# Performance work log

Hardware: AMD Instinct MI355X
Metric: run time of the kernel (lower is better)

Reference implementation:

```python
import jax, jax.numpy as jnp
import numpy as np

DIM_INPUT = 100000
DIM_LATENT = 128
NNZ = 819200
BATCH = 16384


def setup_inputs() -> dict:
    key = jax.random.key(0)
    k1, k2, k3, k4, k5 = jax.random.split(key, 5)
    vals = jax.random.uniform(k1, (NNZ,), dtype=jnp.float32)
    row_idx = jnp.sort(jax.random.randint(k2, (NNZ,), 0, BATCH, dtype=jnp.int32))
    col_idx = jax.random.randint(k3, (NNZ,), 0, DIM_INPUT, dtype=jnp.int32)
    # learned parameters (match torch init: w0 zeros, w/v randn)
    w0 = jnp.zeros((1,), dtype=jnp.float32)
    w = jax.random.normal(k4, (DIM_INPUT,), dtype=jnp.float32)
    v = jax.random.normal(k5, (DIM_INPUT, DIM_LATENT), dtype=jnp.float32)
    return {"vals": vals, "row_idx": row_idx, "col_idx": col_idx,
            "batch": BATCH, "w0": w0, "w": w, "v": v}


def reference(vals, row_idx, col_idx, batch, w0, w, v):
    # x is a sparse [batch, dim_input] matrix in COO form (row_idx, col_idx, vals).
    # linear term: w0 + x @ w
    linear = w0[0] + jax.ops.segment_sum(vals * w[col_idx], row_idx,
                                         num_segments=batch)
    # gather latent rows once: [nnz, K]
    v_rows = v[col_idx]
    weighted = vals[:, None] * v_rows                      # [nnz, K]
    xv = jax.ops.segment_sum(weighted, row_idx, num_segments=batch)       # [B, K]
    x_v_sq = jax.ops.segment_sum(weighted * v_rows, row_idx,
                                 num_segments=batch)       # x @ (v**2): [B, K]
    interaction = 0.5 * (jnp.sum(xv * xv, axis=1) - jnp.sum(x_v_sq, axis=1))
    return linear + interaction
```

## Files before the change

kernel.cpp:

```cpp
#include <hip/hip_runtime.h>

#define FM_NNZ   819200
#define FM_BATCH 16384
#define FM_DIM   100000
#define FM_K     128
#define WAVES    4
#define BATCH    16


static __device__ __forceinline__ uint32_t f2bf(float f) {
    uint32_t u = __float_as_uint(f);
    return (u + 0x7fffu + ((u >> 16) & 1u)) >> 16;
}

__global__ __launch_bounds__(256) void cvt_kernel(const float* __restrict__ v,
                                                  uint32_t* __restrict__ vb) {
    const float4* __restrict__ v4 = (const float4*)v;
    uint2* __restrict__ o = (uint2*)vb;
    const int n = (FM_DIM * FM_K) / 4;
    for (int i = blockIdx.x * blockDim.x + threadIdx.x; i < n;
         i += gridDim.x * blockDim.x) {
        const float4 x = v4[i];
        uint2 r;
        r.x = f2bf(x.x) | (f2bf(x.y) << 16);
        r.y = f2bf(x.z) | (f2bf(x.w) << 16);
        o[i] = r;
    }
}


__global__ __launch_bounds__(256) void fm_fwd_kernel(
    const float* __restrict__ vals,
    const int*   __restrict__ row_idx,
    const int*   __restrict__ col_idx,
    const float* __restrict__ w0,
    const float* __restrict__ w,
    const uint32_t* __restrict__ vb,
    float*       __restrict__ out)
{
    const int wave = threadIdx.x >> 6;
    const int lane = threadIdx.x & 63;
    const int row  = blockIdx.x * WAVES + wave;

    int lo = 0, hi = FM_NNZ;
    while (lo < hi) {
        int mid = (lo + hi) >> 1;
        if (row_idx[mid] < row) lo = mid + 1; else hi = mid;
    }
    const int start = lo;
    hi = FM_NNZ;
    while (lo < hi) {
        int mid = (lo + hi) >> 1;
        if (row_idx[mid] < row + 1) lo = mid + 1; else hi = mid;
    }
    const int end = lo;

    float xv_lo = 0.f, xv_hi = 0.f;
    float sq_lo = 0.f, sq_hi = 0.f;
    float lin = 0.f;

    for (int base = start; base < end; base += 64) {
        const int cnt = min(64, end - base);

        const int idxc = min(base + lane, FM_NNZ - 1);
        const int   c  = col_idx[idxc];
        const float a  = (lane < cnt) ? vals[idxc] : 0.f;

        lin = fmaf(a, w[c], lin);

        int j = 0;
        for (; j + BATCH <= cnt; j += BATCH) {
            uint32_t vv[BATCH];
            float    aa[BATCH];
            #pragma unroll
            for (int u = 0; u < BATCH; ++u) {
                const int cj = __shfl(c, j + u);
                aa[u] = __shfl(a, j + u);
                vv[u] = vb[(size_t)cj * 64 + lane];
            }
            #pragma unroll
            for (int u = 0; u < BATCH; ++u) {
                const float vlo = __uint_as_float(vv[u] << 16);
                const float vhi = __uint_as_float(vv[u] & 0xffff0000u);
                const float tl = aa[u] * vlo;
                const float th = aa[u] * vhi;
                xv_lo += tl;  xv_hi += th;
                sq_lo = fmaf(tl, vlo, sq_lo);
                sq_hi = fmaf(th, vhi, sq_hi);
            }
        }
        for (; j < cnt; ++j) {
            const int   cj = __shfl(c, j);
            const float aj = __shfl(a, j);
            const uint32_t u = vb[(size_t)cj * 64 + lane];
            const float vlo = __uint_as_float(u << 16);
            const float vhi = __uint_as_float(u & 0xffff0000u);
            const float tl = aj * vlo;
            const float th = aj * vhi;
            xv_lo += tl;  xv_hi += th;
            sq_lo = fmaf(tl, vlo, sq_lo);
            sq_hi = fmaf(th, vhi, sq_hi);
        }
    }

    float part = xv_lo * xv_lo + xv_hi * xv_hi - sq_lo - sq_hi;
    #pragma unroll
    for (int off = 32; off > 0; off >>= 1) {
        part += __shfl_down(part, off);
        lin  += __shfl_down(lin,  off);
    }
    if (lane == 0) {
        out[row] = w0[0] + lin + 0.5f * part;
    }
}

extern "C" void kernel_launch(void* const* d_in, const int* in_sizes, int n_in,
                              void* d_out, int out_size, void* d_ws, size_t ws_size,
                              hipStream_t stream) {
    const float* vals    = (const float*)d_in[0];
    const int*   row_idx = (const int*)  d_in[1];
    const int*   col_idx = (const int*)  d_in[2];
    const float* w0      = (const float*)d_in[4];
    const float* w       = (const float*)d_in[5];
    const float* v       = (const float*)d_in[6];
    float*       out     = (float*)d_out;
    uint32_t*    vb      = (uint32_t*)d_ws;

    cvt_kernel<<<1024, 256, 0, stream>>>(v, vb);
    fm_fwd_kernel<<<FM_BATCH / WAVES, 64 * WAVES, 0, stream>>>(
        vals, row_idx, col_idx, w0, w, vb, out);
}
```

Baseline: 165.4 us.

## Split wave into four 16-lane groups loading 16-byte bf16 rows per nonzero

```diff
diff --git a/kernel.cpp b/kernel.cpp
--- a/kernel.cpp
+++ b/kernel.cpp
@@ -5,7 +5,7 @@
 #define FM_DIM   100000
 #define FM_K     128
 #define WAVES    4
-#define BATCH    16
+#define UNR      8
 
 
 static __device__ __forceinline__ uint32_t f2bf(float f) {
@@ -40,6 +40,8 @@
 {
     const int wave = threadIdx.x >> 6;
     const int lane = threadIdx.x & 63;
+    const int grp  = lane >> 4;
+    const int ql   = lane & 15;
     const int row  = blockIdx.x * WAVES + wave;
 
     int lo = 0, hi = FM_NNZ;
@@ -55,8 +57,10 @@
     }
     const int end = lo;
 
-    float xv_lo = 0.f, xv_hi = 0.f;
-    float sq_lo = 0.f, sq_hi = 0.f;
+    const uint4* __restrict__ vb4 = (const uint4*)vb;
+
+    float xv[8] = {0.f,0.f,0.f,0.f,0.f,0.f,0.f,0.f};
+    float sq[8] = {0.f,0.f,0.f,0.f,0.f,0.f,0.f,0.f};
     float lin = 0.f;
 
     for (int base = start; base < end; base += 64) {
@@ -68,42 +72,51 @@
 
         lin = fmaf(a, w[c], lin);
 
-        int j = 0;
-        for (; j + BATCH <= cnt; j += BATCH) {
-            uint32_t vv[BATCH];
-            float    aa[BATCH];
+        for (int j = 0; j < cnt; j += 4 * UNR) {
+            uint4 vv[UNR];
+            float aa[UNR];
             #pragma unroll
-            for (int u = 0; u < BATCH; ++u) {
-                const int cj = __shfl(c, j + u);
-                aa[u] = __shfl(a, j + u);
-                vv[u] = vb[(size_t)cj * 64 + lane];
+            for (int u = 0; u < UNR; ++u) {
+                const int g  = j + 4 * u + grp;
+                const int gc = min(g, cnt - 1);
+                const float av = __shfl(a, gc);
+                const int   cj = __shfl(c, gc);
+                aa[u] = (g < cnt) ? av : 0.f;
+                vv[u] = vb4[(size_t)cj * 16 + ql];
             }
+            __builtin_amdgcn_sched_barrier(0);
             #pragma unroll
-            for (int u = 0; u < BATCH; ++u) {
-                const float vlo = __uint_as_float(vv[u] << 16);
-                const float vhi = __uint_as_float(vv[u] & 0xffff0000u);
-                const float tl = aa[u] * vlo;
-                const float th = aa[u] * vhi;
-                xv_lo += tl;  xv_hi += th;
-                sq_lo = fmaf(tl, vlo, sq_lo);
-                sq_hi = fmaf(th, vhi, sq_hi);
+            for (int u = 0; u < UNR; ++u) {
+                const float au = aa[u];
+                const uint32_t wds[4] = {vv[u].x, vv[u].y, vv[u].z, vv[u].w};
+                #pragma unroll
+                for (int q = 0; q < 4; ++q) {
+                    const float vlo = __uint_as_float(wds[q] << 16);
+                    const float vhi = __uint_as_float(wds[q] & 0xffff0000u);
+                    const float tl  = au * vlo;
+                    const float th  = au * vhi;
+                    xv[2*q]   += tl;
+                    xv[2*q+1] += th;
+                    sq[2*q]   = fmaf(tl, vlo, sq[2*q]);
+                    sq[2*q+1] = fmaf(th, vhi, sq[2*q+1]);
+                }
             }
-        }
-        for (; j < cnt; ++j) {
-            const int   cj = __shfl(c, j);
-            const float aj = __shfl(a, j);
-            const uint32_t u = vb[(size_t)cj * 64 + lane];
-            const float vlo = __uint_as_float(u << 16);
-            const float vhi = __uint_as_float(u & 0xffff0000u);
-            const float tl = aj * vlo;
-            const float th = aj * vhi;
-            xv_lo += tl;  xv_hi += th;
-            sq_lo = fmaf(tl, vlo, sq_lo);
-            sq_hi = fmaf(th, vhi, sq_hi);
         }
     }
 
-    float part = xv_lo * xv_lo + xv_hi * xv_hi - sq_lo - sq_hi;
+    float px = 0.f;
+    #pragma unroll
+    for (int d = 0; d < 8; ++d) {
+        float t = xv[d];
+        t += __shfl_xor(t, 16);
+        t += __shfl_xor(t, 32);
+        px = fmaf(t, t, px);
+    }
+    float sqs = 0.f;
+    #pragma unroll
+    for (int d = 0; d < 8; ++d) sqs += sq[d];
+
+    float part = ((lane < 16) ? px : 0.f) - sqs;
     #pragma unroll
     for (int off = 32; off > 0; off >>= 1) {
         part += __shfl_down(part, off);
```

Measured after the change: 174.9 us. +5.7%, slower.

## Walk column-bucketed nonzeros so concurrent waves share L2-resident latent rows

Applied to the files above, without the earlier changes.

```diff
diff --git a/kernel.cpp b/kernel.cpp
--- a/kernel.cpp
+++ b/kernel.cpp
@@ -4,8 +4,9 @@
 #define FM_BATCH 16384
 #define FM_DIM   100000
 #define FM_K     128
-#define WAVES    4
-#define BATCH    16
+#define NB_SHIFT 13
+#define NBUCK    13
+#define BAD_COL  (1 << 20)
 
 
 static __device__ __forceinline__ uint32_t f2bf(float f) {
@@ -29,88 +30,88 @@
 }
 
 
-__global__ __launch_bounds__(256) void fm_fwd_kernel(
+__global__ __launch_bounds__(256, 8) void fm_fwd_kernel(
     const float* __restrict__ vals,
     const int*   __restrict__ row_idx,
     const int*   __restrict__ col_idx,
     const float* __restrict__ w0,
-    const float* __restrict__ w,
+    const float* __restrict__ w_,
     const uint32_t* __restrict__ vb,
     float*       __restrict__ out)
 {
     const int wave = threadIdx.x >> 6;
     const int lane = threadIdx.x & 63;
-    const int row  = blockIdx.x * WAVES + wave;
+    const int wid  = blockIdx.x * 4 + wave;
+    const int row0 = 2 * wid;
+    const int row1 = row0 + 1;
 
-    int lo = 0, hi = FM_NNZ;
-    while (lo < hi) {
-        int mid = (lo + hi) >> 1;
-        if (row_idx[mid] < row) lo = mid + 1; else hi = mid;
+    int s[3];
+    #pragma unroll
+    for (int q = 0; q < 3; ++q) {
+        const int key = row0 + q;
+        int lo = 0, hi = FM_NNZ;
+        while (lo < hi) {
+            const int mid = (lo + hi) >> 1;
+            if (row_idx[mid] < key) lo = mid + 1; else hi = mid;
+        }
+        s[q] = lo;
     }
-    const int start = lo;
-    hi = FM_NNZ;
-    while (lo < hi) {
-        int mid = (lo + hi) >> 1;
-        if (row_idx[mid] < row + 1) lo = mid + 1; else hi = mid;
-    }
-    const int end = lo;
+    const int s0 = s[0], s1 = s[1], s2 = s[2];
 
-    float xv_lo = 0.f, xv_hi = 0.f;
-    float sq_lo = 0.f, sq_hi = 0.f;
-    float lin = 0.f;
-
-    for (int base = start; base < end; base += 64) {
-        const int cnt = min(64, end - base);
-
-        const int idxc = min(base + lane, FM_NNZ - 1);
-        const int   c  = col_idx[idxc];
-        const float a  = (lane < cnt) ? vals[idxc] : 0.f;
-
-        lin = fmaf(a, w[c], lin);
-
-        int j = 0;
-        for (; j + BATCH <= cnt; j += BATCH) {
-            uint32_t vv[BATCH];
-            float    aa[BATCH];
-            #pragma unroll
-            for (int u = 0; u < BATCH; ++u) {
-                const int cj = __shfl(c, j + u);
-                aa[u] = __shfl(a, j + u);
-                vv[u] = vb[(size_t)cj * 64 + lane];
-            }
-            #pragma unroll
-            for (int u = 0; u < BATCH; ++u) {
-                const float vlo = __uint_as_float(vv[u] << 16);
-                const float vhi = __uint_as_float(vv[u] & 0xffff0000u);
-                const float tl = aa[u] * vlo;
-                const float th = aa[u] * vhi;
-                xv_lo += tl;  xv_hi += th;
-                sq_lo = fmaf(tl, vlo, sq_lo);
-                sq_hi = fmaf(th, vhi, sq_hi);
-            }
-        }
-        for (; j < cnt; ++j) {
-            const int   cj = __shfl(c, j);
-            const float aj = __shfl(a, j);
-            const uint32_t u = vb[(size_t)cj * 64 + lane];
-            const float vlo = __uint_as_float(u << 16);
-            const float vhi = __uint_as_float(u & 0xffff0000u);
-            const float tl = aj * vlo;
-            const float th = aj * vhi;
-            xv_lo += tl;  xv_hi += th;
-            sq_lo = fmaf(tl, vlo, sq_lo);
-            sq_hi = fmaf(th, vhi, sq_hi);
-        }
+    int   cA, cB, cC, cD;
+    float aA, aB, aC, aD;
+    {
+        int idx, ic; bool ok;
+        idx = s0 + lane;      ok = idx < s1; ic = min(idx, FM_NNZ - 1);
+        cA = ok ? col_idx[ic] : BAD_COL;  aA = ok ? vals[ic] : 0.f;
+        idx = s0 + 64 + lane; ok = idx < s1; ic = min(idx, FM_NNZ - 1);
+        cB = ok ? col_idx[ic] : BAD_COL;  aB = ok ? vals[ic] : 0.f;
+        idx = s1 + lane;      ok = idx < s2; ic = min(idx, FM_NNZ - 1);
+        cC = ok ? col_idx[ic] : BAD_COL;  aC = ok ? vals[ic] : 0.f;
+        idx = s1 + 64 + lane; ok = idx < s2; ic = min(idx, FM_NNZ - 1);
+        cD = ok ? col_idx[ic] : BAD_COL;  aD = ok ? vals[ic] : 0.f;
     }
 
-    float part = xv_lo * xv_lo + xv_hi * xv_hi - sq_lo - sq_hi;
+    float xv0l = 0.f, xv0h = 0.f, sq0l = 0.f, sq0h = 0.f, lin0 = 0.f;
+    float xv1l = 0.f, xv1h = 0.f, sq1l = 0.f, sq1h = 0.f, lin1 = 0.f;
+
+#define WALK(creg, areg, xlo, xhi, slo, shi, linr)                         \
+    {                                                                      \
+        unsigned long long m = __ballot(((creg) >> NB_SHIFT) == p);        \
+        while (m) {                                                        \
+            const int j = __ffsll((unsigned long long)m) - 1;              \
+            m &= m - 1;                                                    \
+            const int   cj = __shfl((creg), j);                            \
+            const float aj = __shfl((areg), j);                            \
+            const uint32_t u = vb[(size_t)cj * 64 + lane];                 \
+            linr = fmaf(aj, w_[cj], linr);             \
+            const float vlo = __uint_as_float(u << 16);                    \
+            const float vhi = __uint_as_float(u & 0xffff0000u);            \
+            const float tl = aj * vlo, th = aj * vhi;                      \
+            xlo += tl;  xhi += th;                                         \
+            slo = fmaf(tl, vlo, slo);  shi = fmaf(th, vhi, shi);           \
+        }                                                                  \
+    }
+
+    for (int p = 0; p < NBUCK; ++p) {
+        WALK(cA, aA, xv0l, xv0h, sq0l, sq0h, lin0)
+        WALK(cB, aB, xv0l, xv0h, sq0l, sq0h, lin0)
+        WALK(cC, aC, xv1l, xv1h, sq1l, sq1h, lin1)
+        WALK(cD, aD, xv1l, xv1h, sq1l, sq1h, lin1)
+    }
+#undef WALK
+
+    float part0 = xv0l * xv0l + xv0h * xv0h - sq0l - sq0h;
+    float part1 = xv1l * xv1l + xv1h * xv1h - sq1l - sq1h;
     #pragma unroll
     for (int off = 32; off > 0; off >>= 1) {
-        part += __shfl_down(part, off);
-        lin  += __shfl_down(lin,  off);
+        part0 += __shfl_down(part0, off);
+        part1 += __shfl_down(part1, off);
     }
     if (lane == 0) {
-        out[row] = w0[0] + lin + 0.5f * part;
+        const float bias = w0[0];
+        out[row0] = bias + lin0 + 0.5f * part0;
+        out[row1] = bias + lin1 + 0.5f * part1;
     }
 }
 
@@ -127,6 +128,6 @@
     uint32_t*    vb      = (uint32_t*)d_ws;
 
     cvt_kernel<<<1024, 256, 0, stream>>>(v, vb);
-    fm_fwd_kernel<<<FM_BATCH / WAVES, 64 * WAVES, 0, stream>>>(
+    fm_fwd_kernel<<<FM_BATCH / 8, 256, 0, stream>>>(
         vals, row_idx, col_idx, w0, w, vb, out);
 }
```

Result: slower. 174.7 us (+5.7%).
